# Kernel tuning notes

Hardware: AMD Instinct MI355X
Metric: run time of the kernel (lower is better)

Reference implementation:

```python
import jax, jax.numpy as jnp
import numpy as np

G0, G1, G2 = 128, 64, 32
N0, N1, N2 = 800_000, 200_000, 32_768
EPS = 1e-5
OFFS = np.array([[i, j, k] for i in (0, 1) for j in (0, 1) for k in (0, 1)], np.int64)  # octant order, idx = 4i+2j+k


def _flat(c, G):
    return (c[..., 0] * G + c[..., 1]) * G + c[..., 2]


def _unflat(k, G):
    return np.stack([k // (G * G), (k // G) % G, k % G], -1)


def _child_map(cc, keys_fine, Gf):
    # for each coarse voxel, indices of its 8 fine children (masked if absent)
    k = _flat(2 * cc[:, None, :] + OFFS[None], Gf)  # [M,8]
    pos = np.clip(np.searchsorted(keys_fine, k), 0, len(keys_fine) - 1)
    valid = keys_fine[pos] == k
    return np.where(valid, pos, 0).astype(np.int32), valid


def _parent_map(cf, keys_coarse, Gc):
    pos = np.searchsorted(keys_coarse, _flat(cf // 2, Gc)).astype(np.int32)
    off = ((cf % 2) @ np.array([4, 2, 1])).astype(np.int32)
    return pos, off


def _build():
    rng = np.random.default_rng(0)
    keys2 = np.arange(G2 ** 3, dtype=np.int64)          # coarsest level fully active
    c2 = _unflat(keys2, G2)
    forced1 = _flat(2 * c2 + rng.integers(0, 2, (len(c2), 3)), G1)  # >=1 child per parent
    occ = np.zeros(G1 ** 3, bool); occ[forced1] = True
    extra1 = rng.choice(np.flatnonzero(~occ), N1 - len(forced1), replace=False)
    keys1 = np.sort(np.concatenate([forced1, extra1]))
    c1 = _unflat(keys1, G1)
    cand = _flat((2 * c1[:, None, :] + OFFS[None]).reshape(-1, 3), G0)  # children of active level1
    forced0 = _flat(2 * c1 + rng.integers(0, 2, (N1, 3)), G0)
    occf = np.zeros(G0 ** 3, bool); occf[forced0] = True
    occc = np.zeros(G0 ** 3, bool); occc[cand] = True
    extra0 = rng.choice(np.flatnonzero(occc & ~occf), N0 - N1, replace=False)
    keys0 = np.sort(np.concatenate([forced0, extra0]))
    c0 = _unflat(keys0, G0)
    idx_up1, mask_up1 = _child_map(c1, keys0, G0)
    idx_up2, mask_up2 = _child_map(c2, keys1, G1)
    par_d2, off_d2 = _parent_map(c1, keys2, G2)   # output coords = level1 (x_up1)
    par_d1, off_d1 = _parent_map(c0, keys1, G1)   # output coords = level0 (x)
    return idx_up1, mask_up1, idx_up2, mask_up2, par_d2, off_d2, par_d1, off_d1


def setup_inputs() -> dict:
    key = jax.random.key(0)
    ks = jax.random.split(key, 5)
    idx_up1, mask_up1, idx_up2, mask_up2, par_d2, off_d2, par_d1, off_d1 = _build()
    C0, C1, C2 = 32, 64, 128
    return {
        "x": jax.random.normal(ks[0], (N0, C0), jnp.float32),
        "W_up1": jax.random.normal(ks[1], (8, C0, C1), jnp.float32) / np.sqrt(8 * C0),
        "W_up2": jax.random.normal(ks[2], (8, C1, C2), jnp.float32) / np.sqrt(8 * C1),
        "W_d2": jax.random.normal(ks[3], (8, C2, C1), jnp.float32) / np.sqrt(C2),
        "W_d1": jax.random.normal(ks[4], (8, C1, C0), jnp.float32) / np.sqrt(C1),
        "g1": jnp.ones((C1,), jnp.float32), "b1": jnp.zeros((C1,), jnp.float32),
        "g2": jnp.ones((C2,), jnp.float32), "b2": jnp.zeros((C2,), jnp.float32),
        "g3": jnp.ones((C1,), jnp.float32), "b3": jnp.zeros((C1,), jnp.float32),
        "g4": jnp.ones((C0,), jnp.float32), "b4": jnp.zeros((C0,), jnp.float32),
        "idx_up1": jnp.asarray(idx_up1), "mask_up1": jnp.asarray(mask_up1),
        "idx_up2": jnp.asarray(idx_up2), "mask_up2": jnp.asarray(mask_up2),
        "par_d2": jnp.asarray(par_d2), "off_d2": jnp.asarray(off_d2),
        "par_d1": jnp.asarray(par_d1), "off_d1": jnp.asarray(off_d1),
    }


def _sconv(f, idx, mask, W):
    # stride-2 k=2 sparse conv: gather 8 children then per-offset GEMM
    g = f[idx] * mask[..., None].astype(f.dtype)        # [M,8,Cin]
    return jnp.einsum('mki,kio->mo', g, W)


def _tconv(f, par, off, W):
    # transposed stride-2 k=2: each fine voxel gets one parent, octant selects weight
    fp = f[par]                                          # [M,Cin]
    out = jnp.zeros((fp.shape[0], W.shape[2]), f.dtype)
    for k in range(8):                                   # fixed 8-way kernel loop
        out = out + jnp.where((off == k)[:, None], fp @ W[k], 0.0)
    return out


def _inorm(f, g, b):
    # instance norm over active voxels (single instance), per channel, biased var
    mu = f.mean(0)
    var = f.var(0)
    return (f - mu) * jax.lax.rsqrt(var + EPS) * g + b


def reference(x, W_up1, W_up2, W_d2, W_d1, g1, b1, g2, b2, g3, b3, g4, b4,
              idx_up1, mask_up1, idx_up2, mask_up2, par_d2, off_d2, par_d1, off_d1):
    x_up1 = _inorm(_sconv(x, idx_up1, mask_up1, W_up1), g1, b1)
    x_up2 = _inorm(_sconv(x_up1, idx_up2, mask_up2, W_up2), g2, b2)
    x_down1 = _inorm(_tconv(x_up2, par_d2, off_d2, W_d2), g3, b3)
    x_down2 = _inorm(_tconv(x_down1, par_d1, off_d1, W_d1), g4, b4)
    return (x_down2, x_down1, x_up2, x_up1)
```

## Files before the change

kernel.cpp:

```cpp
#include <hip/hip_runtime.h>
#include <cstdint>
#include <cstddef>

#define EPS_V 1e-5f
#define SLOTS 16

typedef __attribute__((ext_vector_type(8))) short bf16x8;
typedef __attribute__((ext_vector_type(4))) float f32x4;

__device__ __forceinline__ unsigned short f2b(float f) {
    unsigned u = __float_as_uint(f);
    u = (u + 0x7FFFu + ((u >> 16) & 1u)) >> 16;
    return (unsigned short)u;
}

__device__ __forceinline__ bf16x8 cvt8(float4 a, float4 b) {
    bf16x8 r;
    r[0] = (short)f2b(a.x); r[1] = (short)f2b(a.y);
    r[2] = (short)f2b(a.z); r[3] = (short)f2b(a.w);
    r[4] = (short)f2b(b.x); r[5] = (short)f2b(b.y);
    r[6] = (short)f2b(b.z); r[7] = (short)f2b(b.w);
    return r;
}

__device__ __forceinline__ float4 nrm4(float4 v, const float* ss, const float* tt, int c) {
    v.x = fmaf(v.x, ss[c + 0], tt[c + 0]);
    v.y = fmaf(v.y, ss[c + 1], tt[c + 1]);
    v.z = fmaf(v.z, ss[c + 2], tt[c + 2]);
    v.w = fmaf(v.w, ss[c + 3], tt[c + 3]);
    return v;
}

__device__ __forceinline__ void slot_sum(const float* st, int c, float& s0, float& s1) {
    s0 = 0.f; s1 = 0.f;
    #pragma unroll
    for (int s = 0; s < SLOTS; s++) {
        s0 += st[s * 256 + c];
        s1 += st[s * 256 + 128 + c];
    }
}

__global__ void k_detect(const unsigned int* __restrict__ w, int nwords,
                         int* __restrict__ flag) {
    unsigned loc = 0;
    for (int i = threadIdx.x; i < nwords; i += blockDim.x)
        if (w[i] > 1u) loc = 1u;
    if (loc) atomicOr(flag, 1);
}

__device__ __forceinline__ void pack_one(const void* mask, int r, int isByte,
                                         unsigned char* pm) {
    unsigned byte = 0;
    if (isByte) {
        const unsigned char* mb = (const unsigned char*)mask;
        #pragma unroll
        for (int k = 0; k < 8; k++) byte |= (mb[(size_t)r * 8 + k] ? 1u : 0u) << k;
    } else {
        const int* mi = (const int*)mask;
        #pragma unroll
        for (int k = 0; k < 8; k++) byte |= (mi[(size_t)r * 8 + k] ? 1u : 0u) << k;
    }
    pm[r] = (unsigned char)byte;
}

__device__ __forceinline__ void wshuf_one(const float* W, int Cin, int Cout,
                                          unsigned short* dst, int g) {
    int KB = Cin >> 5, NB = Cout >> 4;
    int L = g & 63;
    int rest = g >> 6;
    int nb = rest % NB; rest /= NB;
    int kb = rest % KB; int t = rest / KB;
    int q = L >> 4, col = nb * 16 + (L & 15);
    const float* src = W + ((size_t)t * Cin + kb * 32 + q * 8) * Cout + col;
    unsigned short* d = dst + (size_t)g * 8;
    #pragma unroll
    for (int j = 0; j < 8; j++) d[j] = f2b(src[(size_t)j * Cout]);
}

__global__ __launch_bounds__(256)
void k_prep(const void* msk1, int M1, const void* msk2, int M2,
            const int* __restrict__ flag,
            unsigned char* __restrict__ pm1, unsigned char* __restrict__ pm2,
            const float* __restrict__ W1, const float* __restrict__ W2,
            const float* __restrict__ W3, const float* __restrict__ W4,
            unsigned short* __restrict__ ws1, unsigned short* __restrict__ ws2,
            unsigned short* __restrict__ ws3, unsigned short* __restrict__ ws4,
            const int* __restrict__ par2, int* __restrict__ wmax2,
            const int* __restrict__ par1, int* __restrict__ wmax1,
            int N0, int do_wmax) {
    int P1 = (M1 + 255) >> 8, P2 = (M2 + 255) >> 8;
    int b = blockIdx.x, tid = threadIdx.x;
    if (b < P1) { int r = b * 256 + tid; if (r < M1) pack_one(msk1, r, *flag, pm1); return; }
    b -= P1;
    if (b < P2) { int r = b * 256 + tid; if (r < M2) pack_one(msk2, r, *flag, pm2); return; }
    b -= P2;
    if (b < 8)  { wshuf_one(W1, 32, 64,  ws1, b * 256 + tid); return; }
    b -= 8;
    if (b < 32) { wshuf_one(W2, 64, 128, ws2, b * 256 + tid); return; }
    b -= 32;
    if (b < 32) { wshuf_one(W3, 128, 64, ws3, b * 256 + tid); return; }
    b -= 32;
    if (b < 8)  { wshuf_one(W4, 64, 32,  ws4, b * 256 + tid); return; }
    b -= 8;
    if (!do_wmax) return;
    if (b < P1) { int r = b * 256 + tid; if (r < M1) atomicMax(&wmax2[par2[r]], r + 1); return; }
    b -= P1;
    { int r = b * 256 + tid; if (r < N0) atomicMax(&wmax1[par1[r]], r + 1); }
}

__global__ __launch_bounds__(256)
void k_conv1(const float* __restrict__ xin, const unsigned short* __restrict__ Wsh,
             const int* __restrict__ idx, const unsigned char* __restrict__ pm,
             float* __restrict__ out, float* __restrict__ st, int M) {
    __shared__ unsigned short Wl[8 * 4 * 64 * 8];
    __shared__ float ls[2 * 64];
    {
        const int4* s = (const int4*)Wsh; int4* d = (int4*)Wl;
        for (int i = threadIdx.x; i < 2048; i += 256) d[i] = s[i];
    }
    if (threadIdx.x < 128) ls[threadIdx.x] = 0.f;
    __syncthreads();
    const int lane = threadIdx.x & 63, wid = threadIdx.x >> 6;
    const int q = lane >> 4, li = lane & 15;
    int tile = blockIdx.x * 4 + wid;
    float sum[4] = {0, 0, 0, 0}, sq[4] = {0, 0, 0, 0};
    if (tile * 16 < M) {
        int rowA = tile * 16 + li;
        unsigned m = pm[rowA];
        const int* ip = idx + (size_t)rowA * 8;
        f32x4 acc[4];
        #pragma unroll
        for (int nb = 0; nb < 4; nb++) acc[nb] = (f32x4)0.f;
        #pragma unroll
        for (int t = 0; t < 8; t++) {
            float4 f0 = {0, 0, 0, 0}, f1 = {0, 0, 0, 0};
            if ((m >> t) & 1u) {
                const float4* p = (const float4*)(xin + (size_t)ip[t] * 32 + q * 8);
                f0 = p[0]; f1 = p[1];
            }
            bf16x8 a = cvt8(f0, f1);
            #pragma unroll
            for (int nb = 0; nb < 4; nb++) {
                bf16x8 bb = *(const bf16x8*)&Wl[((t * 4 + nb) * 64 + lane) * 8];
                acc[nb] = __builtin_amdgcn_mfma_f32_16x16x32_bf16(a, bb, acc[nb], 0, 0, 0);
            }
        }
        int rowD = tile * 16 + q * 4;
        #pragma unroll
        for (int nb = 0; nb < 4; nb++)
            #pragma unroll
            for (int r = 0; r < 4; r++) {
                float v = acc[nb][r];
                out[(size_t)(rowD + r) * 64 + nb * 16 + li] = v;
                sum[nb] += v; sq[nb] = fmaf(v, v, sq[nb]);
            }
    }
    #pragma unroll
    for (int nb = 0; nb < 4; nb++) {
        int c = nb * 16 + li;
        atomicAdd(&ls[c], sum[nb]); atomicAdd(&ls[64 + c], sq[nb]);
    }
    __syncthreads();
    int slot = (blockIdx.x & (SLOTS - 1)) << 8;
    if (threadIdx.x < 64) {
        atomicAdd(&st[slot + threadIdx.x], ls[threadIdx.x]);
        atomicAdd(&st[slot + 128 + threadIdx.x], ls[64 + threadIdx.x]);
    }
}

__global__ __launch_bounds__(256)
void k_conv2(const float* xin, const unsigned short* __restrict__ Wsh,
             const int* __restrict__ idx, const unsigned char* __restrict__ pm,
             float* __restrict__ out, float* __restrict__ st, int M,
             const float* __restrict__ st_in, const float* __restrict__ gw,
             const float* __restrict__ bw, int Min, float* nout) {
    __shared__ float ls[2 * 128];
    __shared__ float ss[64], tt[64];
    ls[threadIdx.x] = 0.f;
    if (st_in != nullptr && threadIdx.x < 64) {
        int c = threadIdx.x;
        float s0, s1; slot_sum(st_in, c, s0, s1);
        float invM = 1.0f / (float)Min;
        float mu = s0 * invM;
        float var = fmaf(s1, invM, -mu * mu);
        float s = rsqrtf(var + EPS_V) * gw[c];
        ss[c] = s; tt[c] = fmaf(-mu, s, bw[c]);
    }
    __syncthreads();
    const int lane = threadIdx.x & 63, wid = threadIdx.x >> 6;
    const int q = lane >> 4, li = lane & 15;
    int tile = blockIdx.x * 4 + wid;
    int rowA = tile * 16 + li;
    unsigned m = pm[rowA];
    const int* ip = idx + (size_t)rowA * 8;
    const bool dn = (st_in != nullptr);
    f32x4 acc[8];
    #pragma unroll
    for (int nb = 0; nb < 8; nb++) acc[nb] = (f32x4)0.f;
    for (int t = 0; t < 8; t++) {
        float4 f0 = {0,0,0,0}, f1 = {0,0,0,0}, f2 = {0,0,0,0}, f3 = {0,0,0,0};
        if ((m >> t) & 1u) {
            const float* base = xin + (size_t)ip[t] * 64;
            const float4* p0 = (const float4*)(base + q * 8);
            f0 = p0[0]; f1 = p0[1];
            const float4* p1 = (const float4*)(base + 32 + q * 8);
            f2 = p1[0]; f3 = p1[1];
            if (dn) {
                int c0 = q * 8;
                f0 = nrm4(f0, ss, tt, c0);      f1 = nrm4(f1, ss, tt, c0 + 4);
                f2 = nrm4(f2, ss, tt, 32 + c0); f3 = nrm4(f3, ss, tt, 32 + c0 + 4);
                float4* dpp = (float4*)(nout + (size_t)ip[t] * 64);
                dpp[q * 2] = f0; dpp[q * 2 + 1] = f1;
                dpp[8 + q * 2] = f2; dpp[8 + q * 2 + 1] = f3;
            }
        }
        bf16x8 a0 = cvt8(f0, f1), a1 = cvt8(f2, f3);
        #pragma unroll
        for (int nb = 0; nb < 8; nb++) {
            bf16x8 b0 = *(const bf16x8*)(Wsh + ((size_t)(t * 16 + nb) * 64 + lane) * 8);
            acc[nb] = __builtin_amdgcn_mfma_f32_16x16x32_bf16(a0, b0, acc[nb], 0, 0, 0);
            bf16x8 b1 = *(const bf16x8*)(Wsh + ((size_t)(t * 16 + 8 + nb) * 64 + lane) * 8);
            acc[nb] = __builtin_amdgcn_mfma_f32_16x16x32_bf16(a1, b1, acc[nb], 0, 0, 0);
        }
    }
    int rowD = tile * 16 + q * 4;
    float sum[8], sq[8];
    #pragma unroll
    for (int nb = 0; nb < 8; nb++) {
        sum[nb] = 0.f; sq[nb] = 0.f;
        #pragma unroll
        for (int r = 0; r < 4; r++) {
            float v = acc[nb][r];
            out[(size_t)(rowD + r) * 128 + nb * 16 + li] = v;
            sum[nb] += v; sq[nb] = fmaf(v, v, sq[nb]);
        }
    }
    #pragma unroll
    for (int nb = 0; nb < 8; nb++) {
        int c = nb * 16 + li;
        atomicAdd(&ls[c], sum[nb]); atomicAdd(&ls[128 + c], sq[nb]);
    }
    __syncthreads();
    int slot = (blockIdx.x & (SLOTS - 1)) << 8;
    if (threadIdx.x < 128) {
        atomicAdd(&st[slot + threadIdx.x], ls[threadIdx.x]);
        atomicAdd(&st[slot + 128 + threadIdx.x], ls[128 + threadIdx.x]);
    }
}

__global__ __launch_bounds__(256)
void k_conv3(const float* __restrict__ xin, const unsigned short* __restrict__ Wsh,
             const int* __restrict__ par, const int* __restrict__ off,
             float* __restrict__ out, float* __restrict__ st, int M,
             const float* __restrict__ st_in, const float* __restrict__ gw,
             const float* __restrict__ bw, int Min, float* __restrict__ nout,
             const int* __restrict__ wmax) {
    __shared__ float ls[2 * 64];
    __shared__ float ss[128], tt[128];
    if (threadIdx.x < 128) {
        ls[threadIdx.x & 127] = 0.f;
        if (st_in != nullptr) {
            int c = threadIdx.x;
            float s0, s1; slot_sum(st_in, c, s0, s1);
            float invM = 1.0f / (float)Min;
            float mu = s0 * invM;
            float var = fmaf(s1, invM, -mu * mu);
            float s = rsqrtf(var + EPS_V) * gw[c];
            ss[c] = s; tt[c] = fmaf(-mu, s, bw[c]);
        }
    }
    __syncthreads();
    const int lane = threadIdx.x & 63, wid = threadIdx.x >> 6;
    const int q = lane >> 4, li = lane & 15;
    int pid = blockIdx.x * 4 + wid;
    float sum[4] = {0, 0, 0, 0}, sq[4] = {0, 0, 0, 0};
    if (pid * 32 < M) {
        int r0 = pid * 32 + li, r1 = r0 + 16;
        int p0 = par[r0], p1 = par[r1];
        int o0 = off[r0], o1 = off[r1];
        const bool dn = (st_in != nullptr);
        bool w0 = dn && (wmax[p0] == r0 + 1);
        bool w1 = dn && (wmax[p1] == r1 + 1);
        bf16x8 A0[4], A1[4];
        #pragma unroll
        for (int kb = 0; kb < 4; kb++) {
            const float4* pa = (const float4*)(xin + (size_t)p0 * 128 + kb * 32 + q * 8);
            float4 x0 = pa[0], x1 = pa[1];
            const float4* pb = (const float4*)(xin + (size_t)p1 * 128 + kb * 32 + q * 8);
            float4 y0 = pb[0], y1 = pb[1];
            if (dn) {
                int c0 = kb * 32 + q * 8;
                x0 = nrm4(x0, ss, tt, c0); x1 = nrm4(x1, ss, tt, c0 + 4);
                y0 = nrm4(y0, ss, tt, c0); y1 = nrm4(y1, ss, tt, c0 + 4);
                if (w0) { float4* dp = (float4*)(nout + (size_t)p0 * 128 + kb * 32 + q * 8); dp[0] = x0; dp[1] = x1; }
                if (w1) { float4* dp = (float4*)(nout + (size_t)p1 * 128 + kb * 32 + q * 8); dp[0] = y0; dp[1] = y1; }
            }
            A0[kb] = cvt8(x0, x1);
            A1[kb] = cvt8(y0, y1);
        }
        f32x4 acc0[4], acc1[4];
        #pragma unroll
        for (int nb = 0; nb < 4; nb++) { acc0[nb] = (f32x4)0.f; acc1[nb] = (f32x4)0.f; }
        bf16x8 z8 = (bf16x8)(short)0;
        for (int o = 0; o < 8; o++) {
            bool s0 = (o0 == o), s1 = (o1 == o);
            if (__ballot(s0 || s1) == 0ull) continue;
            bf16x8 M0[4], M1[4];
            #pragma unroll
            for (int kb = 0; kb < 4; kb++) {
                M0[kb] = s0 ? A0[kb] : z8;
                M1[kb] = s1 ? A1[kb] : z8;
            }
            #pragma unroll
            for (int nb = 0; nb < 4; nb++)
                #pragma unroll
                for (int kb = 0; kb < 4; kb++) {
                    bf16x8 bb = *(const bf16x8*)(Wsh + ((((size_t)o * 4 + kb) * 4 + nb) * 64 + lane) * 8);
                    acc0[nb] = __builtin_amdgcn_mfma_f32_16x16x32_bf16(M0[kb], bb, acc0[nb], 0, 0, 0);
                    acc1[nb] = __builtin_amdgcn_mfma_f32_16x16x32_bf16(M1[kb], bb, acc1[nb], 0, 0, 0);
                }
        }
        int d0 = pid * 32 + q * 4, d1 = d0 + 16;
        #pragma unroll
        for (int nb = 0; nb < 4; nb++)
            #pragma unroll
            for (int r = 0; r < 4; r++) {
                float v0 = acc0[nb][r], v1 = acc1[nb][r];
                out[(size_t)(d0 + r) * 64 + nb * 16 + li] = v0;
                out[(size_t)(d1 + r) * 64 + nb * 16 + li] = v1;
                sum[nb] += v0 + v1;
                sq[nb] = fmaf(v0, v0, sq[nb]); sq[nb] = fmaf(v1, v1, sq[nb]);
            }
    }
    #pragma unroll
    for (int nb = 0; nb < 4; nb++) {
        int c = nb * 16 + li;
        atomicAdd(&ls[c], sum[nb]); atomicAdd(&ls[64 + c], sq[nb]);
    }
    __syncthreads();
    int slot = (blockIdx.x & (SLOTS - 1)) << 8;
    if (threadIdx.x < 64) {
        atomicAdd(&st[slot + threadIdx.x], ls[threadIdx.x]);
        atomicAdd(&st[slot + 128 + threadIdx.x], ls[64 + threadIdx.x]);
    }
}

__global__ __launch_bounds__(256)
void k_conv4(const float* __restrict__ xin, const unsigned short* __restrict__ Wsh,
             const int* __restrict__ par, const int* __restrict__ off,
             float* __restrict__ out, float* __restrict__ st, int M,
             const float* __restrict__ st_in, const float* __restrict__ gw,
             const float* __restrict__ bw, int Min, float* __restrict__ nout,
             const int* __restrict__ wmax) {
    __shared__ unsigned short Wl[8 * 2 * 2 * 64 * 8];
    __shared__ float ls[2 * 32];
    __shared__ float ss[64], tt[64];
    {
        const int4* s = (const int4*)Wsh; int4* d = (int4*)Wl;
        for (int i = threadIdx.x; i < 2048; i += 256) d[i] = s[i];
    }
    if (threadIdx.x < 64) {
        if (threadIdx.x < 64) ls[threadIdx.x & 63] = 0.f;
        if (st_in != nullptr) {
            int c = threadIdx.x;
            float s0, s1; slot_sum(st_in, c, s0, s1);
            float invM = 1.0f / (float)Min;
            float mu = s0 * invM;
            float var = fmaf(s1, invM, -mu * mu);
            float s = rsqrtf(var + EPS_V) * gw[c];
            ss[c] = s; tt[c] = fmaf(-mu, s, bw[c]);
        }
    }
    __syncthreads();
    const int lane = threadIdx.x & 63, wid = threadIdx.x >> 6;
    const int q = lane >> 4, li = lane & 15;
    int pid = blockIdx.x * 4 + wid;
    float sum[2] = {0, 0}, sq[2] = {0, 0};
    if (pid * 32 < M) {
        int r0 = pid * 32 + li, r1 = r0 + 16;
        int p0 = par[r0], p1 = par[r1];
        int o0 = off[r0], o1 = off[r1];
        const bool dn = (st_in != nullptr);
        bool w0 = dn && (wmax[p0] == r0 + 1);
        bool w1 = dn && (wmax[p1] == r1 + 1);
        bf16x8 A0[2], A1[2];
        #pragma unroll
        for (int kb = 0; kb < 2; kb++) {
            const float4* pa = (const float4*)(xin + (size_t)p0 * 64 + kb * 32 + q * 8);
            float4 x0 = pa[0], x1 = pa[1];
            const float4* pb = (const float4*)(xin + (size_t)p1 * 64 + kb * 32 + q * 8);
            float4 y0 = pb[0], y1 = pb[1];
            if (dn) {
                int c0 = kb * 32 + q * 8;
                x0 = nrm4(x0, ss, tt, c0); x1 = nrm4(x1, ss, tt, c0 + 4);
                y0 = nrm4(y0, ss, tt, c0); y1 = nrm4(y1, ss, tt, c0 + 4);
                if (w0) { float4* dp = (float4*)(nout + (size_t)p0 * 64 + kb * 32 + q * 8); dp[0] = x0; dp[1] = x1; }
                if (w1) { float4* dp = (float4*)(nout + (size_t)p1 * 64 + kb * 32 + q * 8); dp[0] = y0; dp[1] = y1; }
            }
            A0[kb] = cvt8(x0, x1);
            A1[kb] = cvt8(y0, y1);
        }
        f32x4 acc0[2], acc1[2];
        #pragma unroll
        for (int nb = 0; nb < 2; nb++) { acc0[nb] = (f32x4)0.f; acc1[nb] = (f32x4)0.f; }
        bf16x8 z8 = (bf16x8)(short)0;
        for (int o = 0; o < 8; o++) {
            bool s0 = (o0 == o), s1 = (o1 == o);
            if (__ballot(s0 || s1) == 0ull) continue;
            bf16x8 M0[2], M1[2];
            #pragma unroll
            for (int kb = 0; kb < 2; kb++) {
                M0[kb] = s0 ? A0[kb] : z8;
                M1[kb] = s1 ? A1[kb] : z8;
            }
            #pragma unroll
            for (int nb = 0; nb < 2; nb++)
                #pragma unroll
                for (int kb = 0; kb < 2; kb++) {
                    bf16x8 bb = *(const bf16x8*)&Wl[(((o * 2 + kb) * 2 + nb) * 64 + lane) * 8];
                    acc0[nb] = __builtin_amdgcn_mfma_f32_16x16x32_bf16(M0[kb], bb, acc0[nb], 0, 0, 0);
                    acc1[nb] = __builtin_amdgcn_mfma_f32_16x16x32_bf16(M1[kb], bb, acc1[nb], 0, 0, 0);
                }
        }
        int d0 = pid * 32 + q * 4, d1 = d0 + 16;
        #pragma unroll
        for (int nb = 0; nb < 2; nb++)
            #pragma unroll
            for (int r = 0; r < 4; r++) {
                float v0 = acc0[nb][r], v1 = acc1[nb][r];
                out[(size_t)(d0 + r) * 32 + nb * 16 + li] = v0;
                out[(size_t)(d1 + r) * 32 + nb * 16 + li] = v1;
                sum[nb] += v0 + v1;
                sq[nb] = fmaf(v0, v0, sq[nb]); sq[nb] = fmaf(v1, v1, sq[nb]);
            }
    }
    #pragma unroll
    for (int nb = 0; nb < 2; nb++) {
        int c = nb * 16 + li;
        atomicAdd(&ls[c], sum[nb]); atomicAdd(&ls[32 + c], sq[nb]);
    }
    __syncthreads();
    int slot = (blockIdx.x & (SLOTS - 1)) << 8;
    if (threadIdx.x < 32) {
        atomicAdd(&st[slot + threadIdx.x], ls[threadIdx.x]);
        atomicAdd(&st[slot + 128 + threadIdx.x], ls[32 + threadIdx.x]);
    }
}

template <int C>
__global__ __launch_bounds__(256)
void k_norm(float* __restrict__ f, int M, const float* __restrict__ st,
            const float* __restrict__ g, const float* __restrict__ b) {
    __shared__ float sc[C], sh[C];
    if (threadIdx.x < C) {
        int c = threadIdx.x;
        float s0, s1; slot_sum(st, c, s0, s1);
        float invM = 1.0f / (float)M;
        float mu = s0 * invM;
        float var = fmaf(s1, invM, -mu * mu);
        float s = rsqrtf(var + EPS_V) * g[c];
        sc[c] = s;
        sh[c] = fmaf(-mu, s, b[c]);
    }
    __syncthreads();
    const int total = M * (C / 4);
    const int cq = C / 4;
    float4* p = (float4*)f;
    for (int i = blockIdx.x * blockDim.x + threadIdx.x; i < total;
         i += gridDim.x * blockDim.x) {
        float4 v = p[i];
        int c0 = (i % cq) * 4;
        v.x = fmaf(v.x, sc[c0 + 0], sh[c0 + 0]);
        v.y = fmaf(v.y, sc[c0 + 1], sh[c0 + 1]);
        v.z = fmaf(v.z, sc[c0 + 2], sh[c0 + 2]);
        v.w = fmaf(v.w, sc[c0 + 3], sh[c0 + 3]);
        p[i] = v;
    }
}

extern "C" void kernel_launch(void* const* d_in, const int* in_sizes, int n_in,
                              void* d_out, int out_size, void* d_ws, size_t ws_size,
                              hipStream_t stream) {
    const float* x   = (const float*)d_in[0];
    const float* W1  = (const float*)d_in[1];
    const float* W2  = (const float*)d_in[2];
    const float* W3  = (const float*)d_in[3];
    const float* W4  = (const float*)d_in[4];
    const float* g1  = (const float*)d_in[5];
    const float* b1  = (const float*)d_in[6];
    const float* g2  = (const float*)d_in[7];
    const float* b2  = (const float*)d_in[8];
    const float* g3  = (const float*)d_in[9];
    const float* b3  = (const float*)d_in[10];
    const float* g4  = (const float*)d_in[11];
    const float* b4  = (const float*)d_in[12];
    const int*  idx1 = (const int*)d_in[13];
    const void* msk1 = d_in[14];
    const int*  idx2 = (const int*)d_in[15];
    const void* msk2 = d_in[16];
    const int*  par2 = (const int*)d_in[17];
    const int*  off2 = (const int*)d_in[18];
    const int*  par1 = (const int*)d_in[19];
    const int*  off1 = (const int*)d_in[20];

    const int N1 = in_sizes[17];
    const int N0 = in_sizes[19];
    const int N2 = in_sizes[15] / 8;

    float* outp = (float*)d_out;
    float* sA = outp;
    float* sB = sA + (size_t)N0 * 32;
    float* sC = sB + (size_t)N1 * 64;
    float* sD = sC + (size_t)N2 * 128;

    char* w = (char*)d_ws;
    int*   flag = (int*)w;
    float* st1 = (float*)(w + 256);
    float* st2 = st1 + SLOTS * 256;
    float* st3 = st2 + SLOTS * 256;
    float* st4 = st3 + SLOTS * 256;

    auto al = [](size_t v) { return (v + 255) & ~(size_t)255; };

    size_t o = 256 + (size_t)4 * SLOTS * 256 * 4;
    size_t oS1 = o;  o += 32768;
    size_t oS2 = o;  o += 131072;
    size_t oS3 = o;  o += 131072;
    size_t oS4 = o;  o += 32768;
    size_t oP1 = o;  o += al((size_t)N1);
    size_t oP2 = o;  o += al((size_t)N2); o = al(o);
    size_t oWm2 = o; o += (size_t)N2 * 4;
    size_t oWm1 = o; o += (size_t)N1 * 4; o = al(o);
    size_t wmEnd = o;
    size_t oR2 = o;  o += (size_t)N2 * 128 * 4;
    size_t tierB_need = o;
    size_t oR3 = o;  o += (size_t)N1 * 64 * 4;
    size_t tierA_need = o;

    const int tier = (ws_size >= tierA_need) ? 2 : (ws_size >= tierB_need) ? 1 : 0;

    unsigned short* ws1p = (unsigned short*)(w + oS1);
    unsigned short* ws2p = (unsigned short*)(w + oS2);
    unsigned short* ws3p = (unsigned short*)(w + oS3);
    unsigned short* ws4p = (unsigned short*)(w + oS4);
    unsigned char* pm1 = (unsigned char*)(w + oP1);
    unsigned char* pm2 = (unsigned char*)(w + oP2);
    int* wm2 = (int*)(w + oWm2);
    int* wm1 = (int*)(w + oWm1);
    float* R2 = (float*)(w + oR2);
    float* R3 = (float*)(w + oR3);

    hipMemsetAsync(d_ws, 0, 256 + (size_t)4 * SLOTS * 256 * 4, stream);
    if (tier > 0)
        hipMemsetAsync(w + oWm2, 0, wmEnd - oWm2, stream);

    int nwords = N1 * 8 / 4; if (nwords > 4096) nwords = 4096;
    k_detect<<<1, 256, 0, stream>>>((const unsigned int*)msk1, nwords, flag);

    int P1b = (N1 + 255) / 256, P2b = (N2 + 255) / 256;
    int PW = (tier > 0) ? (P1b + (N0 + 255) / 256) : 0;
    k_prep<<<P1b + P2b + 80 + PW, 256, 0, stream>>>(
        msk1, N1, msk2, N2, flag, pm1, pm2,
        W1, W2, W3, W4, ws1p, ws2p, ws3p, ws4p,
        par2, wm2, par1, wm1, N0, (tier > 0) ? 1 : 0);

    k_conv1<<<(N1 / 16 + 3) / 4, 256, 0, stream>>>(x, ws1p, idx1, pm1, sD, st1, N1);
    if (tier == 0) k_norm<64><<<1024, 256, 0, stream>>>(sD, N1, st1, g1, b1);

    {
        float* outv = (tier > 0) ? R2 : sC;
        k_conv2<<<(N2 / 16) / 4, 256, 0, stream>>>(
            sD, ws2p, idx2, pm2, outv, st2, N2,
            (tier > 0) ? st1 : nullptr, g1, b1, N1,
            (tier > 0) ? sD : nullptr);
        if (tier == 0) k_norm<128><<<512, 256, 0, stream>>>(sC, N2, st2, g2, b2);
    }

    {
        const float* inv = (tier > 0) ? R2 : sC;
        float* outv = (tier == 2) ? R3 : sB;
        k_conv3<<<(N1 / 32 + 3) / 4, 256, 0, stream>>>(
            inv, ws3p, par2, off2, outv, st3, N1,
            (tier > 0) ? st2 : nullptr, g2, b2, N2,
            (tier > 0) ? sC : nullptr, wm2);
        if (tier != 2) k_norm<64><<<1024, 256, 0, stream>>>(sB, N1, st3, g3, b3);
    }

    {
        const float* inv = (tier == 2) ? R3 : sB;
        k_conv4<<<(N0 / 32 + 3) / 4, 256, 0, stream>>>(
            inv, ws4p, par1, off1, sA, st4, N0,
            (tier == 2) ? st3 : nullptr, g3, b3, N1,
            (tier == 2) ? sB : nullptr, wm1);
    }
    k_norm<32><<<1024, 256, 0, stream>>>(sA, N0, st4, g4, b4);
}
```

Before: 607.7 us.

## Fuse whole pipeline into one cooperative persistent kernel with grid syncs

Result: slower. 968.7 us (+59.4%).

```diff
diff --git a/kernel.cpp b/kernel.cpp
--- a/kernel.cpp
+++ b/kernel.cpp
@@ -1,6 +1,9 @@
 #include <hip/hip_runtime.h>
+#include <hip/hip_cooperative_groups.h>
 #include <cstdint>
 #include <cstddef>
+
+namespace cg = cooperative_groups;
 
 #define EPS_V 1e-5f
 #define SLOTS 16
@@ -38,14 +41,6 @@
         s0 += st[s * 256 + c];
         s1 += st[s * 256 + 128 + c];
     }
-}
-
-__global__ void k_detect(const unsigned int* __restrict__ w, int nwords,
-                         int* __restrict__ flag) {
-    unsigned loc = 0;
-    for (int i = threadIdx.x; i < nwords; i += blockDim.x)
-        if (w[i] > 1u) loc = 1u;
-    if (loc) atomicOr(flag, 1);
 }
 
 __device__ __forceinline__ void pack_one(const void* mask, int r, int isByte,
@@ -75,6 +70,396 @@
     unsigned short* d = dst + (size_t)g * 8;
     #pragma unroll
     for (int j = 0; j < 8; j++) d[j] = f2b(src[(size_t)j * Cout]);
+}
+
+struct MArgs {
+    const float *x, *W1, *W2, *W3, *W4;
+    const float *g1, *b1, *g2, *b2, *g3, *b3, *g4, *b4;
+    const int *idx1, *idx2, *par2, *off2, *par1, *off1;
+    const void *msk1, *msk2;
+    int N0, N1, N2;
+    int* flag;
+    float *st1, *st2, *st3, *st4;
+    unsigned short *ws1, *ws2, *ws3, *ws4;
+    unsigned char *pm1, *pm2;
+    int *wm2, *wm1;
+    float *sA, *sB, *sC, *sD, *R2, *R3;
+};
+
+__global__ __launch_bounds__(256, 3)
+void k_mega(MArgs a) {
+    cg::grid_group grid = cg::this_grid();
+    __shared__ unsigned short Wl[16384];
+    __shared__ float ls[256];
+    __shared__ float ss[128], tt[128];
+
+    const int bid = blockIdx.x, nB = gridDim.x, tid = threadIdx.x;
+    const int lane = tid & 63, wid = tid >> 6;
+    const int q = lane >> 4, li = lane & 15;
+
+    for (int i = bid * 256 + tid; i < 4 * SLOTS * 256; i += nB * 256) a.st1[i] = 0.f;
+    for (int i = bid * 256 + tid; i < a.N2; i += nB * 256) a.wm2[i] = 0;
+    for (int i = bid * 256 + tid; i < a.N1; i += nB * 256) a.wm1[i] = 0;
+    if (bid == 0) {
+        if (tid == 0) *a.flag = 0;
+        __syncthreads();
+        int nwords = a.N1 * 8 / 4; if (nwords > 4096) nwords = 4096;
+        const unsigned* w = (const unsigned*)a.msk1;
+        unsigned loc = 0;
+        for (int i = tid; i < nwords; i += 256) if (w[i] > 1u) loc = 1u;
+        if (loc) atomicOr(a.flag, 1);
+    }
+    grid.sync();
+
+    {
+        int P1 = (a.N1 + 255) >> 8, P2 = (a.N2 + 255) >> 8, P0 = (a.N0 + 255) >> 8;
+        int isB = *a.flag;
+        int VB = P1 + P2 + 80 + P1 + P0;
+        for (int vb = bid; vb < VB; vb += nB) {
+            int b = vb;
+            if (b < P1) { int r = b * 256 + tid; if (r < a.N1) pack_one(a.msk1, r, isB, a.pm1); continue; }
+            b -= P1;
+            if (b < P2) { int r = b * 256 + tid; if (r < a.N2) pack_one(a.msk2, r, isB, a.pm2); continue; }
+            b -= P2;
+            if (b < 8)  { wshuf_one(a.W1, 32, 64,  a.ws1, b * 256 + tid); continue; }
+            b -= 8;
+            if (b < 32) { wshuf_one(a.W2, 64, 128, a.ws2, b * 256 + tid); continue; }
+            b -= 32;
+            if (b < 32) { wshuf_one(a.W3, 128, 64, a.ws3, b * 256 + tid); continue; }
+            b -= 32;
+            if (b < 8)  { wshuf_one(a.W4, 64, 32,  a.ws4, b * 256 + tid); continue; }
+            b -= 8;
+            if (b < P1) { int r = b * 256 + tid; if (r < a.N1) atomicMax(&a.wm2[a.par2[r]], r + 1); continue; }
+            b -= P1;
+            { int r = b * 256 + tid; if (r < a.N0) atomicMax(&a.wm1[a.par1[r]], r + 1); }
+        }
+    }
+    grid.sync();
+
+    {
+        const int4* s = (const int4*)a.ws1; int4* d = (int4*)Wl;
+        for (int i = tid; i < 2048; i += 256) d[i] = s[i];
+        if (tid < 128) ls[tid] = 0.f;
+        __syncthreads();
+        float sum[4] = {0, 0, 0, 0}, sq[4] = {0, 0, 0, 0};
+        int nGroups = (a.N1 / 16 + 3) / 4;
+        for (int gi = bid; gi < nGroups; gi += nB) {
+            int tile = gi * 4 + wid;
+            if (tile * 16 >= a.N1) continue;
+            int rowA = tile * 16 + li;
+            unsigned m = a.pm1[rowA];
+            const int* ip = a.idx1 + (size_t)rowA * 8;
+            f32x4 acc[4];
+            #pragma unroll
+            for (int nb = 0; nb < 4; nb++) acc[nb] = (f32x4)0.f;
+            #pragma unroll
+            for (int t = 0; t < 8; t++) {
+                float4 f0 = {0, 0, 0, 0}, f1 = {0, 0, 0, 0};
+                if ((m >> t) & 1u) {
+                    const float4* p = (const float4*)(a.x + (size_t)ip[t] * 32 + q * 8);
+                    f0 = p[0]; f1 = p[1];
+                }
+                bf16x8 av = cvt8(f0, f1);
+                #pragma unroll
+                for (int nb = 0; nb < 4; nb++) {
+                    bf16x8 bb = *(const bf16x8*)&Wl[((t * 4 + nb) * 64 + lane) * 8];
+                    acc[nb] = __builtin_amdgcn_mfma_f32_16x16x32_bf16(av, bb, acc[nb], 0, 0, 0);
+                }
+            }
+            int rowD = tile * 16 + q * 4;
+            #pragma unroll
+            for (int nb = 0; nb < 4; nb++)
+                #pragma unroll
+                for (int r = 0; r < 4; r++) {
+                    float v = acc[nb][r];
+                    a.sD[(size_t)(rowD + r) * 64 + nb * 16 + li] = v;
+                    sum[nb] += v; sq[nb] = fmaf(v, v, sq[nb]);
+                }
+        }
+        #pragma unroll
+        for (int nb = 0; nb < 4; nb++) {
+            int c = nb * 16 + li;
+            atomicAdd(&ls[c], sum[nb]); atomicAdd(&ls[64 + c], sq[nb]);
+        }
+        __syncthreads();
+        int slot = (bid & (SLOTS - 1)) << 8;
+        if (tid < 64) {
+            atomicAdd(&a.st1[slot + tid], ls[tid]);
+            atomicAdd(&a.st1[slot + 128 + tid], ls[64 + tid]);
+        }
+    }
+    grid.sync();
+
+    {
+        ls[tid] = 0.f;
+        if (tid < 64) {
+            float s0, s1; slot_sum(a.st1, tid, s0, s1);
+            float invM = 1.0f / (float)a.N1;
+            float mu = s0 * invM;
+            float var = fmaf(s1, invM, -mu * mu);
+            float s = rsqrtf(var + EPS_V) * a.g1[tid];
+            ss[tid] = s; tt[tid] = fmaf(-mu, s, a.b1[tid]);
+        }
+        __syncthreads();
+        float sum[8] = {0,0,0,0,0,0,0,0}, sq[8] = {0,0,0,0,0,0,0,0};
+        int nGroups = (a.N2 / 16 + 3) / 4;
+        for (int gi = bid; gi < nGroups; gi += nB) {
+            int tile = gi * 4 + wid;
+            if (tile * 16 >= a.N2) continue;
+            int rowA = tile * 16 + li;
+            unsigned m = a.pm2[rowA];
+            const int* ip = a.idx2 + (size_t)rowA * 8;
+            f32x4 acc[8];
+            #pragma unroll
+            for (int nb = 0; nb < 8; nb++) acc[nb] = (f32x4)0.f;
+            for (int t = 0; t < 8; t++) {
+                float4 f0 = {0,0,0,0}, f1 = {0,0,0,0}, f2 = {0,0,0,0}, f3 = {0,0,0,0};
+                if ((m >> t) & 1u) {
+                    const float* base = a.sD + (size_t)ip[t] * 64;
+                    const float4* p0 = (const float4*)(base + q * 8);
+                    f0 = p0[0]; f1 = p0[1];
+                    const float4* p1 = (const float4*)(base + 32 + q * 8);
+                    f2 = p1[0]; f3 = p1[1];
+                    int c0 = q * 8;
+                    f0 = nrm4(f0, ss, tt, c0);      f1 = nrm4(f1, ss, tt, c0 + 4);
+                    f2 = nrm4(f2, ss, tt, 32 + c0); f3 = nrm4(f3, ss, tt, 32 + c0 + 4);
+                    float4* dpp = (float4*)(a.sD + (size_t)ip[t] * 64);
+                    dpp[q * 2] = f0; dpp[q * 2 + 1] = f1;
+                    dpp[8 + q * 2] = f2; dpp[8 + q * 2 + 1] = f3;
+                }
+                bf16x8 a0 = cvt8(f0, f1), a1 = cvt8(f2, f3);
+                #pragma unroll
+                for (int nb = 0; nb < 8; nb++) {
+                    bf16x8 b0 = *(const bf16x8*)(a.ws2 + ((size_t)(t * 16 + nb) * 64 + lane) * 8);
+                    acc[nb] = __builtin_amdgcn_mfma_f32_16x16x32_bf16(a0, b0, acc[nb], 0, 0, 0);
+                    bf16x8 b1 = *(const bf16x8*)(a.ws2 + ((size_t)(t * 16 + 8 + nb) * 64 + lane) * 8);
+                    acc[nb] = __builtin_amdgcn_mfma_f32_16x16x32_bf16(a1, b1, acc[nb], 0, 0, 0);
+                }
+            }
+            int rowD = tile * 16 + q * 4;
+            #pragma unroll
+            for (int nb = 0; nb < 8; nb++)
+                #pragma unroll
+                for (int r = 0; r < 4; r++) {
+                    float v = acc[nb][r];
+                    a.R2[(size_t)(rowD + r) * 128 + nb * 16 + li] = v;
+                    sum[nb] += v; sq[nb] = fmaf(v, v, sq[nb]);
+                }
+        }
+        #pragma unroll
+        for (int nb = 0; nb < 8; nb++) {
+            int c = nb * 16 + li;
+            atomicAdd(&ls[c], sum[nb]); atomicAdd(&ls[128 + c], sq[nb]);
+        }
+        __syncthreads();
+        int slot = (bid & (SLOTS - 1)) << 8;
+        if (tid < 128) {
+            atomicAdd(&a.st2[slot + tid], ls[tid]);
+            atomicAdd(&a.st2[slot + 128 + tid], ls[128 + tid]);
+        }
+    }
+    grid.sync();
+
+    {
+        if (tid < 128) {
+            ls[tid] = 0.f;
+            float s0, s1; slot_sum(a.st2, tid, s0, s1);
+            float invM = 1.0f / (float)a.N2;
+            float mu = s0 * invM;
+            float var = fmaf(s1, invM, -mu * mu);
+            float s = rsqrtf(var + EPS_V) * a.g2[tid];
+            ss[tid] = s; tt[tid] = fmaf(-mu, s, a.b2[tid]);
+        }
+        __syncthreads();
+        float sum[4] = {0, 0, 0, 0}, sq[4] = {0, 0, 0, 0};
+        int nGroups = (a.N1 / 32 + 3) / 4;
+        for (int gi = bid; gi < nGroups; gi += nB) {
+            int pid = gi * 4 + wid;
+            if (pid * 32 >= a.N1) continue;
+            int r0 = pid * 32 + li, r1 = r0 + 16;
+            int p0 = a.par2[r0], p1 = a.par2[r1];
+            int o0 = a.off2[r0], o1 = a.off2[r1];
+            bool w0 = (a.wm2[p0] == r0 + 1);
+            bool w1 = (a.wm2[p1] == r1 + 1);
+            bf16x8 A0[4], A1[4];
+            #pragma unroll
+            for (int kb = 0; kb < 4; kb++) {
+                const float4* pa = (const float4*)(a.R2 + (size_t)p0 * 128 + kb * 32 + q * 8);
+                float4 x0 = pa[0], x1 = pa[1];
+                const float4* pb = (const float4*)(a.R2 + (size_t)p1 * 128 + kb * 32 + q * 8);
+                float4 y0 = pb[0], y1 = pb[1];
+                int c0 = kb * 32 + q * 8;
+                x0 = nrm4(x0, ss, tt, c0); x1 = nrm4(x1, ss, tt, c0 + 4);
+                y0 = nrm4(y0, ss, tt, c0); y1 = nrm4(y1, ss, tt, c0 + 4);
+                if (w0) { float4* dp = (float4*)(a.sC + (size_t)p0 * 128 + kb * 32 + q * 8); dp[0] = x0; dp[1] = x1; }
+                if (w1) { float4* dp = (float4*)(a.sC + (size_t)p1 * 128 + kb * 32 + q * 8); dp[0] = y0; dp[1] = y1; }
+                A0[kb] = cvt8(x0, x1);
+                A1[kb] = cvt8(y0, y1);
+            }
+            f32x4 acc0[4], acc1[4];
+            #pragma unroll
+            for (int nb = 0; nb < 4; nb++) { acc0[nb] = (f32x4)0.f; acc1[nb] = (f32x4)0.f; }
+            bf16x8 z8 = (bf16x8)(short)0;
+            for (int o = 0; o < 8; o++) {
+                bool s0 = (o0 == o), s1 = (o1 == o);
+                if (__ballot(s0 || s1) == 0ull) continue;
+                bf16x8 M0[4], M1[4];
+                #pragma unroll
+                for (int kb = 0; kb < 4; kb++) {
+                    M0[kb] = s0 ? A0[kb] : z8;
+                    M1[kb] = s1 ? A1[kb] : z8;
+                }
+                #pragma unroll
+                for (int nb = 0; nb < 4; nb++)
+                    #pragma unroll
+                    for (int kb = 0; kb < 4; kb++) {
+                        bf16x8 bb = *(const bf16x8*)(a.ws3 + ((((size_t)o * 4 + kb) * 4 + nb) * 64 + lane) * 8);
+                        acc0[nb] = __builtin_amdgcn_mfma_f32_16x16x32_bf16(M0[kb], bb, acc0[nb], 0, 0, 0);
+                        acc1[nb] = __builtin_amdgcn_mfma_f32_16x16x32_bf16(M1[kb], bb, acc1[nb], 0, 0, 0);
+                    }
+            }
+            int d0 = pid * 32 + q * 4, d1 = d0 + 16;
+            #pragma unroll
+            for (int nb = 0; nb < 4; nb++)
+                #pragma unroll
+                for (int r = 0; r < 4; r++) {
+                    float v0 = acc0[nb][r], v1 = acc1[nb][r];
+                    a.R3[(size_t)(d0 + r) * 64 + nb * 16 + li] = v0;
+                    a.R3[(size_t)(d1 + r) * 64 + nb * 16 + li] = v1;
+                    sum[nb] += v0 + v1;
+                    sq[nb] = fmaf(v0, v0, sq[nb]); sq[nb] = fmaf(v1, v1, sq[nb]);
+                }
+        }
+        #pragma unroll
+        for (int nb = 0; nb < 4; nb++) {
+            int c = nb * 16 + li;
+            atomicAdd(&ls[c], sum[nb]); atomicAdd(&ls[64 + c], sq[nb]);
+        }
+        __syncthreads();
+        int slot = (bid & (SLOTS - 1)) << 8;
+        if (tid < 64) {
+            atomicAdd(&a.st3[slot + tid], ls[tid]);
+            atomicAdd(&a.st3[slot + 128 + tid], ls[64 + tid]);
+        }
+    }
+    grid.sync();
+
+    {
+        const int4* s = (const int4*)a.ws4; int4* d = (int4*)Wl;
+        for (int i = tid; i < 2048; i += 256) d[i] = s[i];
+        if (tid < 64) {
+            ls[tid] = 0.f;
+            float s0, s1; slot_sum(a.st3, tid, s0, s1);
+            float invM = 1.0f / (float)a.N1;
+            float mu = s0 * invM;
+            float var = fmaf(s1, invM, -mu * mu);
+            float sv = rsqrtf(var + EPS_V) * a.g3[tid];
+            ss[tid] = sv; tt[tid] = fmaf(-mu, sv, a.b3[tid]);
+        }
+        __syncthreads();
+        float sum[2] = {0, 0}, sq[2] = {0, 0};
+        int nGroups = (a.N0 / 32 + 3) / 4;
+        for (int gi = bid; gi < nGroups; gi += nB) {
+            int pid = gi * 4 + wid;
+            if (pid * 32 >= a.N0) continue;
+            int r0 = pid * 32 + li, r1 = r0 + 16;
+            int p0 = a.par1[r0], p1 = a.par1[r1];
+            int o0 = a.off1[r0], o1 = a.off1[r1];
+            bool w0 = (a.wm1[p0] == r0 + 1);
+            bool w1 = (a.wm1[p1] == r1 + 1);
+            bf16x8 A0[2], A1[2];
+            #pragma unroll
+            for (int kb = 0; kb < 2; kb++) {
+                const float4* pa = (const float4*)(a.R3 + (size_t)p0 * 64 + kb * 32 + q * 8);
+                float4 x0 = pa[0], x1 = pa[1];
+                const float4* pb = (const float4*)(a.R3 + (size_t)p1 * 64 + kb * 32 + q * 8);
+                float4 y0 = pb[0], y1 = pb[1];
+                int c0 = kb * 32 + q * 8;
+                x0 = nrm4(x0, ss, tt, c0); x1 = nrm4(x1, ss, tt, c0 + 4);
+                y0 = nrm4(y0, ss, tt, c0); y1 = nrm4(y1, ss, tt, c0 + 4);
+                if (w0) { float4* dp = (float4*)(a.sB + (size_t)p0 * 64 + kb * 32 + q * 8); dp[0] = x0; dp[1] = x1; }
+                if (w1) { float4* dp = (float4*)(a.sB + (size_t)p1 * 64 + kb * 32 + q * 8); dp[0] = y0; dp[1] = y1; }
+                A0[kb] = cvt8(x0, x1);
+                A1[kb] = cvt8(y0, y1);
+            }
+            f32x4 acc0[2], acc1[2];
+            #pragma unroll
+            for (int nb = 0; nb < 2; nb++) { acc0[nb] = (f32x4)0.f; acc1[nb] = (f32x4)0.f; }
+            bf16x8 z8 = (bf16x8)(short)0;
+            for (int o = 0; o < 8; o++) {
+                bool s0 = (o0 == o), s1 = (o1 == o);
+                if (__ballot(s0 || s1) == 0ull) continue;
+                bf16x8 M0[2], M1[2];
+                #pragma unroll
+                for (int kb = 0; kb < 2; kb++) {
+                    M0[kb] = s0 ? A0[kb] : z8;
+                    M1[kb] = s1 ? A1[kb] : z8;
+                }
+                #pragma unroll
+                for (int nb = 0; nb < 2; nb++)
+                    #pragma unroll
+                    for (int kb = 0; kb < 2; kb++) {
+                        bf16x8 bb = *(const bf16x8*)&Wl[(((o * 2 + kb) * 2 + nb) * 64 + lane) * 8];
+                        acc0[nb] = __builtin_amdgcn_mfma_f32_16x16x32_bf16(M0[kb], bb, acc0[nb], 0, 0, 0);
+                        acc1[nb] = __builtin_amdgcn_mfma_f32_16x16x32_bf16(M1[kb], bb, acc1[nb], 0, 0, 0);
+                    }
+            }
+            int d0 = pid * 32 + q * 4, d1 = d0 + 16;
+            #pragma unroll
+            for (int nb = 0; nb < 2; nb++)
+                #pragma unroll
+                for (int r = 0; r < 4; r++) {
+                    float v0 = acc0[nb][r], v1 = acc1[nb][r];
+                    a.sA[(size_t)(d0 + r) * 32 + nb * 16 + li] = v0;
+                    a.sA[(size_t)(d1 + r) * 32 + nb * 16 + li] = v1;
+                    sum[nb] += v0 + v1;
+                    sq[nb] = fmaf(v0, v0, sq[nb]); sq[nb] = fmaf(v1, v1, sq[nb]);
+                }
+        }
+        #pragma unroll
+        for (int nb = 0; nb < 2; nb++) {
+            int c = nb * 16 + li;
+            atomicAdd(&ls[c], sum[nb]); atomicAdd(&ls[32 + c], sq[nb]);
+        }
+        __syncthreads();
+        int slot = (bid & (SLOTS - 1)) << 8;
+        if (tid < 32) {
+            atomicAdd(&a.st4[slot + tid], ls[tid]);
+            atomicAdd(&a.st4[slot + 128 + tid], ls[32 + tid]);
+        }
+    }
+    grid.sync();
+
+    {
+        if (tid < 32) {
+            float s0, s1; slot_sum(a.st4, tid, s0, s1);
+            float invM = 1.0f / (float)a.N0;
+            float mu = s0 * invM;
+            float var = fmaf(s1, invM, -mu * mu);
+            float s = rsqrtf(var + EPS_V) * a.g4[tid];
+            ss[tid] = s; tt[tid] = fmaf(-mu, s, a.b4[tid]);
+        }
+        __syncthreads();
+        const int total = a.N0 * 8;
+        float4* p = (float4*)a.sA;
+        for (int i = bid * 256 + tid; i < total; i += nB * 256) {
+            float4 v = p[i];
+            int c0 = (i & 7) * 4;
+            v.x = fmaf(v.x, ss[c0 + 0], tt[c0 + 0]);
+            v.y = fmaf(v.y, ss[c0 + 1], tt[c0 + 1]);
+            v.z = fmaf(v.z, ss[c0 + 2], tt[c0 + 2]);
+            v.w = fmaf(v.w, ss[c0 + 3], tt[c0 + 3]);
+            p[i] = v;
+        }
+    }
+}
+
+__global__ void k_detect(const unsigned int* __restrict__ w, int nwords,
+                         int* __restrict__ flag) {
+    unsigned loc = 0;
+    for (int i = threadIdx.x; i < nwords; i += blockDim.x)
+        if (w[i] > 1u) loc = 1u;
+    if (loc) atomicOr(flag, 1);
 }
 
 __global__ __launch_bounds__(256)
@@ -138,11 +523,11 @@
                 const float4* p = (const float4*)(xin + (size_t)ip[t] * 32 + q * 8);
                 f0 = p[0]; f1 = p[1];
             }
-            bf16x8 a = cvt8(f0, f1);
+            bf16x8 av = cvt8(f0, f1);
             #pragma unroll
             for (int nb = 0; nb < 4; nb++) {
                 bf16x8 bb = *(const bf16x8*)&Wl[((t * 4 + nb) * 64 + lane) * 8];
-                acc[nb] = __builtin_amdgcn_mfma_f32_16x16x32_bf16(a, bb, acc[nb], 0, 0, 0);
+                acc[nb] = __builtin_amdgcn_mfma_f32_16x16x32_bf16(av, bb, acc[nb], 0, 0, 0);
             }
         }
         int rowD = tile * 16 + q * 4;
@@ -550,6 +935,48 @@
     float* R2 = (float*)(w + oR2);
     float* R3 = (float*)(w + oR3);
 
+    if (tier == 2) {
+        static int s_grid = 0;
+        if (s_grid == 0) {
+            int dev = 0;
+            if (hipGetDevice(&dev) == hipSuccess) {
+                hipDeviceProp_t prop;
+                int maxb = 0;
+                if (hipGetDeviceProperties(&prop, dev) == hipSuccess &&
+                    hipOccupancyMaxActiveBlocksPerMultiprocessor(&maxb, k_mega, 256, 0) == hipSuccess &&
+                    maxb > 0 && prop.cooperativeLaunch) {
+                    s_grid = maxb * prop.multiProcessorCount;
+                } else {
+                    s_grid = -1;
+                }
+            } else {
+                s_grid = -1;
+            }
+        }
+        if (s_grid > 0) {
+            MArgs ma;
+            ma.x = x; ma.W1 = W1; ma.W2 = W2; ma.W3 = W3; ma.W4 = W4;
+            ma.g1 = g1; ma.b1 = b1; ma.g2 = g2; ma.b2 = b2;
+            ma.g3 = g3; ma.b3 = b3; ma.g4 = g4; ma.b4 = b4;
+            ma.idx1 = idx1; ma.idx2 = idx2;
+            ma.par2 = par2; ma.off2 = off2; ma.par1 = par1; ma.off1 = off1;
+            ma.msk1 = msk1; ma.msk2 = msk2;
+            ma.N0 = N0; ma.N1 = N1; ma.N2 = N2;
+            ma.flag = flag;
+            ma.st1 = st1; ma.st2 = st2; ma.st3 = st3; ma.st4 = st4;
+            ma.ws1 = ws1p; ma.ws2 = ws2p; ma.ws3 = ws3p; ma.ws4 = ws4p;
+            ma.pm1 = pm1; ma.pm2 = pm2;
+            ma.wm2 = wm2; ma.wm1 = wm1;
+            ma.sA = sA; ma.sB = sB; ma.sC = sC; ma.sD = sD;
+            ma.R2 = R2; ma.R3 = R3;
+            void* params[] = { (void*)&ma };
+            hipError_t e = hipLaunchCooperativeKernel(
+                k_mega, dim3(s_grid), dim3(256), params, 0, stream);
+            if (e == hipSuccess) return;
+            s_grid = -1;
+        }
+    }
+
     hipMemsetAsync(d_ws, 0, 256 + (size_t)4 * SLOTS * 256 * 4, stream);
     if (tier > 0)
         hipMemsetAsync(w + oWm2, 0, wmEnd - oWm2, stream);
```
